# Optimization experiments

Hardware: AMD Instinct MI355X
Metric: run time of the kernel (lower is better)

The kernel has to match this reference:

```python
import jax, jax.numpy as jnp
import numpy as np

B, S, NX, NH = 4, 1024, 1024, 16
HD = NX // NH  # head_features = 64


def setup_inputs() -> dict:
    key = jax.random.key(0)
    k1, k2, k3 = jax.random.split(key, 3)
    x = jax.random.normal(k1, (B, S, NX), dtype=jnp.float32)
    w_attn = 0.02 * jax.random.normal(k2, (NX, 3 * NX), dtype=jnp.float32)
    b_attn = jnp.zeros((3 * NX,), dtype=jnp.float32)
    w_proj = 0.02 * jax.random.normal(k3, (NX, NX), dtype=jnp.float32)
    b_proj = jnp.zeros((NX,), dtype=jnp.float32)
    causal_bias = jnp.tril(jnp.ones((S, S), dtype=jnp.float32))  # tril buffer
    return {"x": x, "w_attn": w_attn, "b_attn": b_attn,
            "w_proj": w_proj, "b_proj": b_proj, "causal_bias": causal_bias}


def reference(x, w_attn, b_attn, w_proj, b_proj, causal_bias):
    # c_attn: fused qkv projection (Conv1D == addmm)
    qkv = x @ w_attn + b_attn                     # [B, S, 3*NX]
    q, k, v = jnp.split(qkv, 3, axis=-1)          # each [B, S, NX]
    # split heads -> [B, H, S, D]
    q = q.reshape(B, S, NH, HD).transpose(0, 2, 1, 3)
    k = k.reshape(B, S, NH, HD).transpose(0, 2, 1, 3)
    v = v.reshape(B, S, NH, HD).transpose(0, 2, 1, 3)
    # present: stack of (key in [B,H,S,D] layout, value)
    present = jnp.stack((k, v))                   # [2, B, H, S, D]
    # scores with scale=True
    w = jnp.einsum('bhqd,bhkd->bhqk', q, k) / jnp.sqrt(jnp.float32(HD))
    b = causal_bias[None, None, :, :]             # [1,1,S,S] (nd==ns==S)
    w = w * b - 1e10 * (1.0 - b)                  # multiplicative mask trick
    p = jax.nn.softmax(w, axis=-1)
    a = jnp.einsum('bhqk,bhkd->bhqd', p, v)       # [B, H, S, D]
    a = a.transpose(0, 2, 1, 3).reshape(B, S, NX)  # merge heads
    out = a @ w_proj + b_proj                     # c_proj
    return out, present
```

## Files before the change

### kernel.cpp

```cpp
#include <hip/hip_runtime.h>
#include <hip/hip_bf16.h>

typedef __attribute__((ext_vector_type(8))) short short8;
typedef __attribute__((ext_vector_type(4))) float floatx4;

constexpr int Bsz = 4, Ssz = 1024, NXc = 1024, NHc = 16, HDc = 64;
constexpr int OUT_ELEMS  = Bsz * Ssz * NXc;
constexpr int HEAD_ELEMS = Bsz * NHc * Ssz * HDc;

union BF8 { __hip_bfloat16 h[8]; uint4 v; short8 s; };

__device__ __forceinline__ uint4 cvt8(const float* __restrict__ p) {
    float4 a = *reinterpret_cast<const float4*>(p);
    float4 b = *reinterpret_cast<const float4*>(p + 4);
    BF8 u;
    u.h[0] = __float2bfloat16(a.x); u.h[1] = __float2bfloat16(a.y);
    u.h[2] = __float2bfloat16(a.z); u.h[3] = __float2bfloat16(a.w);
    u.h[4] = __float2bfloat16(b.x); u.h[5] = __float2bfloat16(b.y);
    u.h[6] = __float2bfloat16(b.z); u.h[7] = __float2bfloat16(b.w);
    return u.v;
}

__device__ __forceinline__ void load_lds_16B(const void* g, void* l) {
    __builtin_amdgcn_global_load_lds(
        (const __attribute__((address_space(1))) unsigned int*)g,
        (__attribute__((address_space(3))) unsigned int*)l, 16, 0, 0);
}


__global__ __launch_bounds__(256) void prep_kernel(
    const float* __restrict__ x, __hip_bfloat16* __restrict__ x_bf,
    const float* __restrict__ w_attn, __hip_bfloat16* __restrict__ wTa,
    const float* __restrict__ w_proj, __hip_bfloat16* __restrict__ wTp)
{
    const int bid = blockIdx.x, tid = threadIdx.x;
    __shared__ float t[64][65];
    if (bid < 2048) {
        const int i = (bid * 256 + tid) * 8;
        *reinterpret_cast<uint4*>(x_bf + i) = cvt8(x + i);
        return;
    }
    const float* in; __hip_bfloat16* outp; int N, bx, by;
    if (bid < 2816) { const int q = bid - 2048; in = w_attn; outp = wTa; N = 3072; bx = q % 48; by = q / 48; }
    else            { const int q = bid - 2816; in = w_proj; outp = wTp; N = 1024; bx = q % 16; by = q / 16; }
    const int k0 = by * 64, n0 = bx * 64;
#pragma unroll
    for (int j = 0; j < 16; ++j) {
        const int idx = tid + j * 256;
        const int row = idx >> 6, col = idx & 63;
        t[row][col] = in[(size_t)(k0 + row) * N + n0 + col];
    }
    __syncthreads();
#pragma unroll
    for (int j = 0; j < 16; ++j) {
        const int idx = tid + j * 256;
        const int orow = idx >> 6, ocol = idx & 63;
        outp[(size_t)(n0 + orow) * 1024 + k0 + ocol] = __float2bfloat16(t[ocol][orow]);
    }
}

template <int EPI>
__global__ __launch_bounds__(256) void gemm128p(
    const __hip_bfloat16* __restrict__ A,
    const __hip_bfloat16* __restrict__ Bt,
    const float* __restrict__ bias,
    float* __restrict__ outf,
    __hip_bfloat16* __restrict__ qws,
    float* __restrict__ present,
    __hip_bfloat16* __restrict__ kws,
    __hip_bfloat16* __restrict__ vtws,
    int M, int N, int K)
{
    __shared__ __align__(16) __hip_bfloat16 As[3][4096];
    __shared__ __align__(16) __hip_bfloat16 Bs[3][4096];

    const int nbx = N >> 7;
    const int nwg = (M >> 7) * nbx;
    const int wg  = blockIdx.x;
    const int swz = (wg & 7) * (nwg >> 3) + (wg >> 3);
    const int by  = swz / nbx, bx = swz % nbx;

    const int tid  = threadIdx.x;
    const int w    = tid >> 6, lane = tid & 63;
    const int quad = lane >> 4, l16 = lane & 15;
    const int m0 = by * 128, n0 = bx * 128;
    const int mb = (w >> 1) * 64, nbw = (w & 1) * 64;

    const int srow = lane >> 2;
    const int sksw = (((lane & 3) ^ ((lane >> 3) & 3))) * 8;
    const int rsw = (l16 >> 1) & 3;

    floatx4 acc[4][4];
#pragma unroll
    for (int i = 0; i < 4; ++i)
#pragma unroll
        for (int j = 0; j < 4; ++j)
#pragma unroll
            for (int r = 0; r < 4; ++r) acc[i][j][r] = 0.f;

    auto stage = [&](int buf, int k0) {
#pragma unroll
        for (int c = 0; c < 2; ++c) {
            const int chunk = w * 2 + c;
            const int row = chunk * 16 + srow;
            load_lds_16B(A + (size_t)(m0 + row) * K + k0 + sksw,
                         &As[buf][chunk * 512]);
            load_lds_16B(Bt + (size_t)(n0 + row) * K + k0 + sksw,
                         &Bs[buf][chunk * 512]);
        }
    };

    stage(0, 0);
    stage(1, 32);
    int cb = 0;
    for (int k0 = 0; k0 < K; k0 += 32) {
        if (k0 + 32 < K) {
            asm volatile("s_waitcnt vmcnt(4)" ::: "memory");
        } else {
            asm volatile("s_waitcnt vmcnt(0)" ::: "memory");
        }
        __builtin_amdgcn_s_barrier();
        __builtin_amdgcn_sched_barrier(0);

        if (k0 + 64 < K) {
            const int nb_ = (cb >= 1) ? cb - 1 : 2;
            stage(nb_, k0 + 64);
        }

        short8 af[4], bfr[4];
#pragma unroll
        for (int mi = 0; mi < 4; ++mi)
            af[mi] = *reinterpret_cast<const short8*>(
                &As[cb][(mb + mi * 16 + l16) * 32 + ((quad ^ rsw) * 8)]);
#pragma unroll
        for (int ni = 0; ni < 4; ++ni)
            bfr[ni] = *reinterpret_cast<const short8*>(
                &Bs[cb][(nbw + ni * 16 + l16) * 32 + ((quad ^ rsw) * 8)]);
        __builtin_amdgcn_s_setprio(1);
#pragma unroll
        for (int mi = 0; mi < 4; ++mi)
#pragma unroll
            for (int ni = 0; ni < 4; ++ni)
                acc[mi][ni] = __builtin_amdgcn_mfma_f32_16x16x32_bf16(
                    af[mi], bfr[ni], acc[mi][ni], 0, 0, 0);
        __builtin_amdgcn_s_setprio(0);

        cb = (cb == 2) ? 0 : cb + 1;
    }

#pragma unroll
    for (int mi = 0; mi < 4; ++mi) {
#pragma unroll
        for (int ni = 0; ni < 4; ++ni) {
            const int col = n0 + nbw + ni * 16 + l16;
            const float bsv = bias[col];
#pragma unroll
            for (int r = 0; r < 4; ++r) {
                const int row = m0 + mb + mi * 16 + quad * 4 + r;
                const float v = acc[mi][ni][r] + bsv;
                if (EPI == 0) {
                    const int seg = col >> 10;
                    const int c = col & 1023;
                    if (seg == 0) {
                        qws[(size_t)row * 1024 + c] = __float2bfloat16(v);
                    } else {
                        const int bq = row >> 10, s = row & 1023;
                        const int hh = c >> 6, d = c & 63;
                        const size_t idx =
                            ((size_t)((bq * 16 + hh) * 1024 + s)) * 64 + d;
                        const int kt = s >> 6, key = s & 63;
                        const size_t tbase =
                            ((size_t)((bq * 16 + hh) * 16 + kt)) * 4096;
                        if (seg == 1) {
                            present[idx] = v;
                            kws[tbase + key * 64 +
                                ((((d >> 3) ^ (key & 7)) << 3) | (d & 7))] =
                                __float2bfloat16(v);
                        } else {
                            present[HEAD_ELEMS + idx] = v;
                            vtws[tbase + d * 64 +
                                ((((key >> 3) ^ (d & 7)) << 3) | (key & 7))] =
                                __float2bfloat16(v);
                        }
                    }
                } else {
                    outf[(size_t)row * N + col] = v;
                }
            }
        }
    }
}

__global__ __launch_bounds__(256) void gemm_proj(
    const __hip_bfloat16* __restrict__ A,
    const __hip_bfloat16* __restrict__ Bt,
    const float* __restrict__ bias,
    float* __restrict__ outf)
{
    constexpr int K = 1024, N = 1024;
    __shared__ __align__(16) __hip_bfloat16 As[3][4096];
    __shared__ __align__(16) __hip_bfloat16 Bs[3][2048];

    const int wg  = blockIdx.x;
    const int swz = (wg & 7) * 64 + (wg >> 3);
    const int by  = swz >> 4, bx = swz & 15;

    const int tid  = threadIdx.x;
    const int w    = tid >> 6, lane = tid & 63;
    const int quad = lane >> 4, l16 = lane & 15;
    const int m0 = by * 128, n0 = bx * 64;
    const int mbase = w * 32;

    const int srow = lane >> 2;
    const int sksw = (((lane & 3) ^ ((lane >> 3) & 3))) * 8;
    const int rsw = (l16 >> 1) & 3;

    floatx4 acc[2][4];
#pragma unroll
    for (int i = 0; i < 2; ++i)
#pragma unroll
        for (int j = 0; j < 4; ++j)
#pragma unroll
            for (int r = 0; r < 4; ++r) acc[i][j][r] = 0.f;

    auto stage = [&](int buf, int k0) {
#pragma unroll
        for (int c = 0; c < 2; ++c) {
            const int chunk = w * 2 + c;
            const int row = chunk * 16 + srow;
            load_lds_16B(A + (size_t)(m0 + row) * K + k0 + sksw,
                         &As[buf][chunk * 512]);
        }
        const int brow = w * 16 + srow;
        load_lds_16B(Bt + (size_t)(n0 + brow) * K + k0 + sksw,
                     &Bs[buf][w * 512]);
    };

    stage(0, 0);
    stage(1, 32);
    int cb = 0;
    for (int k0 = 0; k0 < K; k0 += 32) {
        if (k0 + 32 < K) {
            asm volatile("s_waitcnt vmcnt(3)" ::: "memory");
        } else {
            asm volatile("s_waitcnt vmcnt(0)" ::: "memory");
        }
        __builtin_amdgcn_s_barrier();
        __builtin_amdgcn_sched_barrier(0);

        if (k0 + 64 < K) {
            const int nb_ = (cb >= 1) ? cb - 1 : 2;
            stage(nb_, k0 + 64);
        }

        short8 af[2], bfr[4];
#pragma unroll
        for (int mi = 0; mi < 2; ++mi)
            af[mi] = *reinterpret_cast<const short8*>(
                &As[cb][(mbase + mi * 16 + l16) * 32 + ((quad ^ rsw) * 8)]);
#pragma unroll
        for (int ni = 0; ni < 4; ++ni)
            bfr[ni] = *reinterpret_cast<const short8*>(
                &Bs[cb][(ni * 16 + l16) * 32 + ((quad ^ rsw) * 8)]);
        __builtin_amdgcn_s_setprio(1);
#pragma unroll
        for (int mi = 0; mi < 2; ++mi)
#pragma unroll
            for (int ni = 0; ni < 4; ++ni)
                acc[mi][ni] = __builtin_amdgcn_mfma_f32_16x16x32_bf16(
                    af[mi], bfr[ni], acc[mi][ni], 0, 0, 0);
        __builtin_amdgcn_s_setprio(0);

        cb = (cb == 2) ? 0 : cb + 1;
    }

#pragma unroll
    for (int mi = 0; mi < 2; ++mi) {
#pragma unroll
        for (int ni = 0; ni < 4; ++ni) {
            const int col = n0 + ni * 16 + l16;
            const float bsv = bias[col];
#pragma unroll
            for (int r = 0; r < 4; ++r) {
                const int row = m0 + mbase + mi * 16 + quad * 4 + r;
                outf[(size_t)row * N + col] = acc[mi][ni][r] + bsv;
            }
        }
    }
}

__global__ __launch_bounds__(256) void attn_v6(
    const __hip_bfloat16* __restrict__ q_ws,
    const __hip_bfloat16* __restrict__ k_ws,
    const __hip_bfloat16* __restrict__ vt_ws,
    __hip_bfloat16* __restrict__ a_ws)
{
    const int wg  = blockIdx.x;
    const int swz = (wg & 7) * 64 + (wg >> 3);
    const int bx  = swz & 7;
    const int bh  = swz >> 3;
    const int b = bh >> 4, h = bh & 15;

    const int tid  = threadIdx.x;
    const int wave = tid >> 6, lane = tid & 63;
    const int quad = lane >> 4, l16 = lane & 15;
    const int stripe = wave * 16;

    const __hip_bfloat16* Kbase = k_ws  + (size_t)bh * 65536;
    const __hip_bfloat16* Vbase = vt_ws + (size_t)bh * 65536;

    __shared__ __align__(16) __hip_bfloat16 Ksf[4][4096];
    __shared__ __align__(16) __hip_bfloat16 Vsf[4][4096];
    __shared__ __align__(16) __hip_bfloat16 Ps[64][72];

    constexpr float SCL = 0.18033688011f;

#pragma unroll
    for (int pass = 0; pass < 2; ++pass) {
        const int qt = (pass == 0) ? (8 + bx) : (7 - bx);

        const __hip_bfloat16* Qb =
            q_ws + ((size_t)(b * Ssz + qt * 64 + stripe + l16)) * NXc + h * 64;
        const short8 qf0 = *reinterpret_cast<const short8*>(Qb + quad * 8);
        const short8 qf1 = *reinterpret_cast<const short8*>(Qb + 32 + quad * 8);

        float m_i[4], l_i[4];
#pragma unroll
        for (int r = 0; r < 4; ++r) { m_i[r] = -1e9f; l_i[r] = 0.f; }
        floatx4 oacc[4];
#pragma unroll
        for (int ni = 0; ni < 4; ++ni)
#pragma unroll
            for (int r = 0; r < 4; ++r) oacc[ni][r] = 0.f;

#pragma unroll
        for (int c2 = 0; c2 < 2; ++c2) {
            const int c = wave + c2 * 4;
            load_lds_16B(Kbase + c * 512 + (lane << 3), &Ksf[0][c * 512]);
            load_lds_16B(Vbase + c * 512 + (lane << 3), &Vsf[0][c * 512]);
        }
        if (qt >= 1) {
#pragma unroll
            for (int c2 = 0; c2 < 2; ++c2) {
                const int c = wave + c2 * 4;
                load_lds_16B(Kbase + 4096 + c * 512 + (lane << 3),
                             &Ksf[1][c * 512]);
                load_lds_16B(Vbase + 4096 + c * 512 + (lane << 3),
                             &Vsf[1][c * 512]);
            }
        }

        for (int kt = 0; kt <= qt; ++kt) {
            const int cw = kt & 3;
            if (kt + 2 <= qt) {
                const int nb_ = (kt + 2) & 3;
                const __hip_bfloat16* Kt = Kbase + (size_t)(kt + 2) * 4096;
                const __hip_bfloat16* Vt = Vbase + (size_t)(kt + 2) * 4096;
#pragma unroll
                for (int c2 = 0; c2 < 2; ++c2) {
                    const int c = wave + c2 * 4;
                    load_lds_16B(Kt + c * 512 + (lane << 3), &Ksf[nb_][c * 512]);
                    load_lds_16B(Vt + c * 512 + (lane << 3), &Vsf[nb_][c * 512]);
                }
                asm volatile("s_waitcnt vmcnt(8)" ::: "memory");
            } else if (kt + 1 <= qt) {
                asm volatile("s_waitcnt vmcnt(4)" ::: "memory");
            } else {
                asm volatile("s_waitcnt vmcnt(0)" ::: "memory");
            }
            __builtin_amdgcn_s_barrier();
            __builtin_amdgcn_sched_barrier(0);

            floatx4 sacc[4];
#pragma unroll
            for (int ni = 0; ni < 4; ++ni)
#pragma unroll
                for (int r = 0; r < 4; ++r) sacc[ni][r] = 0.f;
            __builtin_amdgcn_s_setprio(1);
#pragma unroll
            for (int ni = 0; ni < 4; ++ni) {
                const int key = ni * 16 + l16;
                const int sw = key & 7;
                const short8 kf0 = *reinterpret_cast<const short8*>(
                    &Ksf[cw][key * 64 + ((quad ^ sw) << 3)]);
                const short8 kf1 = *reinterpret_cast<const short8*>(
                    &Ksf[cw][key * 64 + (((4 + quad) ^ sw) << 3)]);
                sacc[ni] = __builtin_amdgcn_mfma_f32_16x16x32_bf16(
                    qf0, kf0, sacc[ni], 0, 0, 0);
                sacc[ni] = __builtin_amdgcn_mfma_f32_16x16x32_bf16(
                    qf1, kf1, sacc[ni], 0, 0, 0);
            }
            __builtin_amdgcn_s_setprio(0);

            const bool diag = (kt == qt);
            float alpha_[4];
#pragma unroll
            for (int r = 0; r < 4; ++r) {
                const int lrow = stripe + quad * 4 + r;
                float sv[4];
                float mx = -1e30f;
#pragma unroll
                for (int ni = 0; ni < 4; ++ni) {
                    float v = sacc[ni][r] * SCL;
                    if (diag && (ni * 16 + l16) > lrow) v = -1e9f;
                    sv[ni] = v;
                    mx = fmaxf(mx, v);
                }
                mx = fmaxf(mx, __shfl_xor(mx, 1));
                mx = fmaxf(mx, __shfl_xor(mx, 2));
                mx = fmaxf(mx, __shfl_xor(mx, 4));
                mx = fmaxf(mx, __shfl_xor(mx, 8));
                const float mnew = fmaxf(m_i[r], mx);
                const float al = exp2f(m_i[r] - mnew);
                m_i[r] = mnew;
                float s = 0.f;
#pragma unroll
                for (int nn = 0; nn < 4; ++nn) {
                    const int ni = (nn + quad) & 3;
                    const float p = exp2f(sv[ni] - mnew);
                    s += p;
                    Ps[lrow][ni * 16 + l16] = __float2bfloat16(p);
                }
                s += __shfl_xor(s, 1);
                s += __shfl_xor(s, 2);
                s += __shfl_xor(s, 4);
                s += __shfl_xor(s, 8);
                l_i[r] = l_i[r] * al + s;
                alpha_[r] = al;
            }

#pragma unroll
            for (int ni = 0; ni < 4; ++ni)
#pragma unroll
                for (int r = 0; r < 4; ++r) oacc[ni][r] *= alpha_[r];

            __builtin_amdgcn_s_setprio(1);
#pragma unroll
            for (int kk = 0; kk < 64; kk += 32) {
                const short8 pf = *reinterpret_cast<const short8*>(
                    &Ps[stripe + l16][kk + quad * 8]);
#pragma unroll
                for (int ni = 0; ni < 4; ++ni) {
                    const int d = ni * 16 + l16;
                    const int chunk = (kk >> 3) + quad;
                    const short8 vf = *reinterpret_cast<const short8*>(
                        &Vsf[cw][d * 64 + ((chunk ^ (d & 7)) << 3)]);
                    oacc[ni] = __builtin_amdgcn_mfma_f32_16x16x32_bf16(
                        pf, vf, oacc[ni], 0, 0, 0);
                }
            }
            __builtin_amdgcn_s_setprio(0);
        }

        __builtin_amdgcn_s_barrier();

#pragma unroll
        for (int ni = 0; ni < 4; ++ni) {
#pragma unroll
            for (int r = 0; r < 4; ++r) {
                const int row = qt * 64 + stripe + quad * 4 + r;
                const int col = h * 64 + ni * 16 + l16;
                const float inv = 1.0f / fmaxf(l_i[r], 1e-20f);
                a_ws[((size_t)(b * Ssz + row)) * NXc + col] =
                    __float2bfloat16(oacc[ni][r] * inv);
            }
        }
    }
}

template <int EPI>
__global__ __launch_bounds__(256) void gemm64(
    const void* __restrict__ Av, const float* __restrict__ Bw,
    const float* __restrict__ bias, float* __restrict__ out0,
    float* __restrict__ present, int M, int N, int K)
{
    __shared__ __align__(16) __hip_bfloat16 As[64][40];
    __shared__ __align__(16) __hip_bfloat16 Bs[64][40];
    const int tid = threadIdx.x;
    const int wave = tid >> 6, lane = tid & 63;
    const int quad = lane >> 4, l16 = lane & 15;
    const int m0 = blockIdx.y * 64, n0 = blockIdx.x * 64;
    const int mb = (wave >> 1) * 32, nb = (wave & 1) * 32;
    const int arow = tid >> 2, aseg = tid & 3;
    const int brow = tid >> 3, bseg = tid & 7;
    floatx4 acc[2][2];
#pragma unroll
    for (int i = 0; i < 2; ++i)
#pragma unroll
        for (int j = 0; j < 2; ++j)
#pragma unroll
            for (int r = 0; r < 4; ++r) acc[i][j][r] = 0.f;
    for (int k0 = 0; k0 < K; k0 += 32) {
        if (EPI == 0) {
            const float* A = (const float*)Av;
            *reinterpret_cast<uint4*>(&As[arow][aseg * 8]) =
                cvt8(A + (size_t)(m0 + arow) * K + k0 + aseg * 8);
        } else {
            const __hip_bfloat16* A = (const __hip_bfloat16*)Av;
            *reinterpret_cast<uint4*>(&As[arow][aseg * 8]) =
                *reinterpret_cast<const uint4*>(
                    A + (size_t)(m0 + arow) * K + k0 + aseg * 8);
        }
        const float* bp = Bw + (size_t)(k0 + brow) * N + n0 + bseg * 8;
        float4 b0 = *reinterpret_cast<const float4*>(bp);
        float4 b1 = *reinterpret_cast<const float4*>(bp + 4);
        Bs[bseg * 8 + 0][brow] = __float2bfloat16(b0.x);
        Bs[bseg * 8 + 1][brow] = __float2bfloat16(b0.y);
        Bs[bseg * 8 + 2][brow] = __float2bfloat16(b0.z);
        Bs[bseg * 8 + 3][brow] = __float2bfloat16(b0.w);
        Bs[bseg * 8 + 4][brow] = __float2bfloat16(b1.x);
        Bs[bseg * 8 + 5][brow] = __float2bfloat16(b1.y);
        Bs[bseg * 8 + 6][brow] = __float2bfloat16(b1.z);
        Bs[bseg * 8 + 7][brow] = __float2bfloat16(b1.w);
        __syncthreads();
        short8 af[2], bf[2];
#pragma unroll
        for (int mm = 0; mm < 2; ++mm)
            af[mm] = *reinterpret_cast<const short8*>(&As[mb + mm * 16 + l16][quad * 8]);
#pragma unroll
        for (int nn = 0; nn < 2; ++nn)
            bf[nn] = *reinterpret_cast<const short8*>(&Bs[nb + nn * 16 + l16][quad * 8]);
#pragma unroll
        for (int mm = 0; mm < 2; ++mm)
#pragma unroll
            for (int nn = 0; nn < 2; ++nn)
                acc[mm][nn] = __builtin_amdgcn_mfma_f32_16x16x32_bf16(
                    af[mm], bf[nn], acc[mm][nn], 0, 0, 0);
        __syncthreads();
    }
#pragma unroll
    for (int mm = 0; mm < 2; ++mm)
#pragma unroll
        for (int nn = 0; nn < 2; ++nn) {
            const int col = n0 + nb + nn * 16 + l16;
            const float bsv = bias[col];
#pragma unroll
            for (int r = 0; r < 4; ++r) {
                const int row = m0 + mb + mm * 16 + quad * 4 + r;
                const float v = acc[mm][nn][r] + bsv;
                if (EPI == 0) {
                    const int seg = col >> 10;
                    const int c = col & 1023;
                    if (seg == 0) out0[(size_t)row * 1024 + c] = v;
                    else {
                        const int b = row >> 10, s = row & 1023;
                        const int h = c >> 6, d = c & 63;
                        const size_t idx = ((size_t)((b * 16 + h) * 1024 + s)) * 64 + d;
                        if (seg == 1) present[idx] = v;
                        else          present[HEAD_ELEMS + idx] = v;
                    }
                } else out0[(size_t)row * N + col] = v;
            }
        }
}

__global__ __launch_bounds__(256) void attn64(
    const float* __restrict__ qbuf, const float* __restrict__ present,
    __hip_bfloat16* __restrict__ a_ws)
{
    const int qt = blockIdx.x, h = blockIdx.y, b = blockIdx.z;
    const int tid = threadIdx.x;
    const int wave = tid >> 6, lane = tid & 63;
    const int quad = lane >> 4, l16 = lane & 15;
    const int mb = (wave >> 1) * 32, nb = (wave & 1) * 32;
    const size_t headoff = ((size_t)(b * 16 + h)) * Ssz * HDc;
    const float* Qb = qbuf + ((size_t)(b * Ssz + qt * 64)) * NXc + h * 64;
    const float* Kp = present + headoff;
    const float* Vp = present + HEAD_ELEMS + headoff;
    __shared__ __align__(16) __hip_bfloat16 Qs[64][72];
    __shared__ __align__(16) __hip_bfloat16 Ks[64][72];
    __shared__ __align__(16) __hip_bfloat16 Vts[64][72];
    __shared__ __align__(16) __hip_bfloat16 Ps[64][72];
    __shared__ float Sc[64][65];
    __shared__ float mrow[64], lrow[64], arw[64];
#pragma unroll
    for (int it = 0; it < 2; ++it) {
        const int c = tid + it * 256;
        const int row = c >> 3, seg = c & 7;
        *reinterpret_cast<uint4*>(&Qs[row][seg * 8]) =
            cvt8(Qb + (size_t)row * NXc + seg * 8);
    }
    if (tid < 64) { mrow[tid] = -1e9f; lrow[tid] = 0.f; }
    floatx4 oacc[2][2];
#pragma unroll
    for (int i = 0; i < 2; ++i)
#pragma unroll
        for (int j = 0; j < 2; ++j)
#pragma unroll
            for (int r = 0; r < 4; ++r) oacc[i][j][r] = 0.f;
    __syncthreads();
    for (int kt = 0; kt <= qt; ++kt) {
#pragma unroll
        for (int it = 0; it < 2; ++it) {
            const int c = tid + it * 256;
            const int row = c >> 3, seg = c & 7;
            *reinterpret_cast<uint4*>(&Ks[row][seg * 8]) =
                cvt8(Kp + (size_t)(kt * 64 + row) * 64 + seg * 8);
            const float* vp = Vp + (size_t)(kt * 64 + row) * 64 + seg * 8;
            float4 v0 = *reinterpret_cast<const float4*>(vp);
            float4 v1 = *reinterpret_cast<const float4*>(vp + 4);
            Vts[seg * 8 + 0][row] = __float2bfloat16(v0.x);
            Vts[seg * 8 + 1][row] = __float2bfloat16(v0.y);
            Vts[seg * 8 + 2][row] = __float2bfloat16(v0.z);
            Vts[seg * 8 + 3][row] = __float2bfloat16(v0.w);
            Vts[seg * 8 + 4][row] = __float2bfloat16(v1.x);
            Vts[seg * 8 + 5][row] = __float2bfloat16(v1.y);
            Vts[seg * 8 + 6][row] = __float2bfloat16(v1.z);
            Vts[seg * 8 + 7][row] = __float2bfloat16(v1.w);
        }
        __syncthreads();
        floatx4 sacc[2][2];
#pragma unroll
        for (int i = 0; i < 2; ++i)
#pragma unroll
            for (int j = 0; j < 2; ++j)
#pragma unroll
                for (int r = 0; r < 4; ++r) sacc[i][j][r] = 0.f;
#pragma unroll
        for (int kd = 0; kd < 64; kd += 32) {
            short8 af[2], bf[2];
#pragma unroll
            for (int mm = 0; mm < 2; ++mm)
                af[mm] = *reinterpret_cast<const short8*>(&Qs[mb + mm * 16 + l16][kd + quad * 8]);
#pragma unroll
            for (int nn = 0; nn < 2; ++nn)
                bf[nn] = *reinterpret_cast<const short8*>(&Ks[nb + nn * 16 + l16][kd + quad * 8]);
#pragma unroll
            for (int mm = 0; mm < 2; ++mm)
#pragma unroll
                for (int nn = 0; nn < 2; ++nn)
                    sacc[mm][nn] = __builtin_amdgcn_mfma_f32_16x16x32_bf16(
                        af[mm], bf[nn], sacc[mm][nn], 0, 0, 0);
        }
        const bool diag = (kt == qt);
#pragma unroll
        for (int mm = 0; mm < 2; ++mm)
#pragma unroll
            for (int nn = 0; nn < 2; ++nn)
#pragma unroll
                for (int r = 0; r < 4; ++r) {
                    const int row = mb + mm * 16 + quad * 4 + r;
                    const int col = nb + nn * 16 + l16;
                    float v = fminf(fmaxf(sacc[mm][nn][r] * 0.125f, -1e8f), 1e8f);
                    if (diag && col > row) v = -1e9f;
                    Sc[row][col] = v;
                }
        __syncthreads();
        if (tid < 64) {
            const int r = tid;
            const float mo = mrow[r];
            float mx = mo;
            for (int c = 0; c < 64; ++c) mx = fmaxf(mx, Sc[r][c]);
            const float al = (mo <= -5e8f) ? 0.f : __expf(mo - mx);
            float sum = 0.f;
            for (int c = 0; c < 64; ++c) {
                const float sv = Sc[r][c];
                const float p = (sv <= -5e8f) ? 0.f : __expf(sv - mx);
                sum += p;
                Ps[r][c] = __float2bfloat16(p);
            }
            mrow[r] = mx;
            lrow[r] = lrow[r] * al + sum;
            arw[r]  = al;
        }
        __syncthreads();
#pragma unroll
        for (int mm = 0; mm < 2; ++mm) {
            const int rbase = mb + mm * 16 + quad * 4;
#pragma unroll
            for (int r = 0; r < 4; ++r) {
                const float al = arw[rbase + r];
                oacc[mm][0][r] *= al;
                oacc[mm][1][r] *= al;
            }
        }
#pragma unroll
        for (int kk = 0; kk < 64; kk += 32) {
            short8 pf[2], vf[2];
#pragma unroll
            for (int mm = 0; mm < 2; ++mm)
                pf[mm] = *reinterpret_cast<const short8*>(&Ps[mb + mm * 16 + l16][kk + quad * 8]);
#pragma unroll
            for (int nn = 0; nn < 2; ++nn)
                vf[nn] = *reinterpret_cast<const short8*>(&Vts[nb + nn * 16 + l16][kk + quad * 8]);
#pragma unroll
            for (int mm = 0; mm < 2; ++mm)
#pragma unroll
                for (int nn = 0; nn < 2; ++nn)
                    oacc[mm][nn] = __builtin_amdgcn_mfma_f32_16x16x32_bf16(
                        pf[mm], vf[nn], oacc[mm][nn], 0, 0, 0);
        }
        __syncthreads();
    }
#pragma unroll
    for (int mm = 0; mm < 2; ++mm)
#pragma unroll
        for (int nn = 0; nn < 2; ++nn)
#pragma unroll
            for (int r = 0; r < 4; ++r) {
                const int row = mb + mm * 16 + quad * 4 + r;
                const int col = nb + nn * 16 + l16;
                const float inv = 1.0f / fmaxf(lrow[row], 1e-20f);
                a_ws[((size_t)(b * Ssz + qt * 64 + row)) * NXc + h * 64 + col] =
                    __float2bfloat16(oacc[mm][nn][r] * inv);
            }
}

extern "C" void kernel_launch(void* const* d_in, const int* in_sizes, int n_in,
                              void* d_out, int out_size, void* d_ws, size_t ws_size,
                              hipStream_t stream) {
    const float* x      = (const float*)d_in[0];
    const float* w_attn = (const float*)d_in[1];
    const float* b_attn = (const float*)d_in[2];
    const float* w_proj = (const float*)d_in[3];
    const float* b_proj = (const float*)d_in[4];

    float* out     = (float*)d_out;
    float* present = out + OUT_ELEMS;

    const size_t NEED = 32u * 1024u * 1024u;
    if (ws_size >= NEED) {
        __hip_bfloat16* reg1 = (__hip_bfloat16*)d_ws;
        __hip_bfloat16* reg2 = reg1 + 4194304;
        __hip_bfloat16* reg3 = reg2 + 4194304;
        __hip_bfloat16* wTa  = reg3 + 4194304;
        __hip_bfloat16* wTp  = wTa + 3145728;
        __hip_bfloat16* kws  = (__hip_bfloat16*)out;
        __hip_bfloat16* vtws = kws + 4194304;

        prep_kernel<<<3072, 256, 0, stream>>>(x, reg1, w_attn, wTa, w_proj, wTp);

        gemm128p<0><<<768, 256, 0, stream>>>(
            reg1, wTa, b_attn, nullptr, reg2, present, kws, vtws,
            4096, 3072, 1024);

        attn_v6<<<512, 256, 0, stream>>>(reg2, kws, vtws, reg2);

        gemm_proj<<<512, 256, 0, stream>>>(reg2, wTp, b_proj, out);
    } else {
        __hip_bfloat16* a_ws = (__hip_bfloat16*)d_ws;
        hipMemsetAsync(d_ws, 0, (size_t)OUT_ELEMS * sizeof(__hip_bfloat16), stream);
        gemm64<0><<<dim3(48, 64), 256, 0, stream>>>(x, w_attn, b_attn, out, present,
                                                    4096, 3072, 1024);
        attn64<<<dim3(16, 16, 4), 256, 0, stream>>>(out, present, a_ws);
        gemm64<1><<<dim3(16, 64), 256, 0, stream>>>(a_ws, w_proj, b_proj, out, nullptr,
                                                    4096, 1024, 1024);
    }
}
```

Measured before the change: 195.9 us.

## Replace QKV GEMM with 256x256-tile, 8-wave kernel and split-phase staging

The QKV projection GEMM moves from 128x128 tiles with 4 waves to 256x256 tiles with 8 waves, each wave computing 128x64. Each K-step is split into two MFMA halves, with the A and B prefetches interleaved between barriers. The aim is more operand reuse per LDS load and better overlap of global-to-LDS traffic with MFMA work. The grid shrinks from 768 to 192 workgroups, which is fewer than the CU count on MI355X, so occupancy and load balance may suffer, and LDS use rises to 96KB per block.

```diff
diff --git a/kernel.cpp b/kernel.cpp
--- a/kernel.cpp
+++ b/kernel.cpp
@@ -59,132 +59,155 @@
     }
 }
 
-template <int EPI>
-__global__ __launch_bounds__(256) void gemm128p(
+__global__ __launch_bounds__(512) void gemm256(
     const __hip_bfloat16* __restrict__ A,
     const __hip_bfloat16* __restrict__ Bt,
     const float* __restrict__ bias,
-    float* __restrict__ outf,
     __hip_bfloat16* __restrict__ qws,
     float* __restrict__ present,
     __hip_bfloat16* __restrict__ kws,
-    __hip_bfloat16* __restrict__ vtws,
-    int M, int N, int K)
+    __hip_bfloat16* __restrict__ vtws)
 {
-    __shared__ __align__(16) __hip_bfloat16 As[3][4096];
-    __shared__ __align__(16) __hip_bfloat16 Bs[3][4096];
-
-    const int nbx = N >> 7;
-    const int nwg = (M >> 7) * nbx;
+    constexpr int K = 1024;
+    __shared__ __align__(16) __hip_bfloat16 As[3][8192];
+    __shared__ __align__(16) __hip_bfloat16 Bs[3][8192];
+
     const int wg  = blockIdx.x;
-    const int swz = (wg & 7) * (nwg >> 3) + (wg >> 3);
-    const int by  = swz / nbx, bx = swz % nbx;
+    const int swz = (wg & 7) * 24 + (wg >> 3);
+    const int by  = swz / 12, bx = swz % 12;
 
     const int tid  = threadIdx.x;
     const int w    = tid >> 6, lane = tid & 63;
+    const int wm   = w >> 2, wn = w & 3;
     const int quad = lane >> 4, l16 = lane & 15;
-    const int m0 = by * 128, n0 = bx * 128;
-    const int mb = (w >> 1) * 64, nbw = (w & 1) * 64;
+    const int m0 = by * 256, n0 = bx * 256;
+    const int mb = wm * 128, nb = wn * 64;
 
     const int srow = lane >> 2;
-    const int sksw = (((lane & 3) ^ ((lane >> 3) & 3))) * 8;
-    const int rsw = (l16 >> 1) & 3;
-
-    floatx4 acc[4][4];
-#pragma unroll
-    for (int i = 0; i < 4; ++i)
+    const int sk   = (((lane & 3) ^ ((lane >> 3) & 3))) * 8;
+    const int rsw  = (l16 >> 1) & 3;
+
+    floatx4 acc[8][4];
+#pragma unroll
+    for (int i = 0; i < 8; ++i)
 #pragma unroll
         for (int j = 0; j < 4; ++j)
 #pragma unroll
             for (int r = 0; r < 4; ++r) acc[i][j][r] = 0.f;
 
-    auto stage = [&](int buf, int k0) {
+    auto stageA = [&](int buf, int k0) {
 #pragma unroll
         for (int c = 0; c < 2; ++c) {
-            const int chunk = w * 2 + c;
-            const int row = chunk * 16 + srow;
-            load_lds_16B(A + (size_t)(m0 + row) * K + k0 + sksw,
-                         &As[buf][chunk * 512]);
-            load_lds_16B(Bt + (size_t)(n0 + row) * K + k0 + sksw,
-                         &Bs[buf][chunk * 512]);
+            const int blk = w * 2 + c;
+            const int row = blk * 16 + srow;
+            load_lds_16B(A + (size_t)(m0 + row) * K + k0 + sk,
+                         &As[buf][blk * 512]);
         }
     };
-
-    stage(0, 0);
-    stage(1, 32);
-    int cb = 0;
-    for (int k0 = 0; k0 < K; k0 += 32) {
-        if (k0 + 32 < K) {
+    auto stageB = [&](int buf, int k0) {
+#pragma unroll
+        for (int c = 0; c < 2; ++c) {
+            const int blk = w * 2 + c;
+            const int row = blk * 16 + srow;
+            load_lds_16B(Bt + (size_t)(n0 + row) * K + k0 + sk,
+                         &Bs[buf][blk * 512]);
+        }
+    };
+
+    stageA(0, 0);  stageB(0, 0);
+    stageA(1, 32); stageB(1, 32);
+    asm volatile("s_waitcnt vmcnt(4)" ::: "memory");
+    __builtin_amdgcn_s_barrier();
+    __builtin_amdgcn_sched_barrier(0);
+
+    for (int t = 0; t < 32; ++t) {
+        const int cb = t % 3;
+        const int k0 = t * 32;
+        const int nbuf = (t + 2) % 3;
+        const int rc = (quad ^ rsw) * 8;
+
+        short8 af0[4], bfr[4];
+#pragma unroll
+        for (int mi = 0; mi < 4; ++mi)
+            af0[mi] = *reinterpret_cast<const short8*>(
+                &As[cb][(mb + mi * 16 + l16) * 32 + rc]);
+#pragma unroll
+        for (int ni = 0; ni < 4; ++ni)
+            bfr[ni] = *reinterpret_cast<const short8*>(
+                &Bs[cb][(nb + ni * 16 + l16) * 32 + rc]);
+        if (t + 2 < 32) stageA(nbuf, k0 + 64);
+        __builtin_amdgcn_s_barrier();
+        __builtin_amdgcn_sched_barrier(0);
+        __builtin_amdgcn_s_setprio(1);
+#pragma unroll
+        for (int mi = 0; mi < 4; ++mi)
+#pragma unroll
+            for (int ni = 0; ni < 4; ++ni)
+                acc[mi][ni] = __builtin_amdgcn_mfma_f32_16x16x32_bf16(
+                    af0[mi], bfr[ni], acc[mi][ni], 0, 0, 0);
+        __builtin_amdgcn_s_setprio(0);
+
+        short8 af1[4];
+#pragma unroll
+        for (int mi = 0; mi < 4; ++mi)
+            af1[mi] = *reinterpret_cast<const short8*>(
+                &As[cb][(mb + 64 + mi * 16 + l16) * 32 + rc]);
+        if (t + 2 < 32) stageB(nbuf, k0 + 64);
+        __builtin_amdgcn_s_barrier();
+        __builtin_amdgcn_sched_barrier(0);
+        __builtin_amdgcn_s_setprio(1);
+#pragma unroll
+        for (int mi = 0; mi < 4; ++mi)
+#pragma unroll
+            for (int ni = 0; ni < 4; ++ni)
+                acc[4 + mi][ni] = __builtin_amdgcn_mfma_f32_16x16x32_bf16(
+                    af1[mi], bfr[ni], acc[4 + mi][ni], 0, 0, 0);
+        __builtin_amdgcn_s_setprio(0);
+
+        if (t + 2 < 32) {
             asm volatile("s_waitcnt vmcnt(4)" ::: "memory");
         } else {
             asm volatile("s_waitcnt vmcnt(0)" ::: "memory");
         }
-        __builtin_amdgcn_s_barrier();
-        __builtin_amdgcn_sched_barrier(0);
-
-        if (k0 + 64 < K) {
-            const int nb_ = (cb >= 1) ? cb - 1 : 2;
-            stage(nb_, k0 + 64);
-        }
-
-        short8 af[4], bfr[4];
-#pragma unroll
-        for (int mi = 0; mi < 4; ++mi)
-            af[mi] = *reinterpret_cast<const short8*>(
-                &As[cb][(mb + mi * 16 + l16) * 32 + ((quad ^ rsw) * 8)]);
-#pragma unroll
-        for (int ni = 0; ni < 4; ++ni)
-            bfr[ni] = *reinterpret_cast<const short8*>(
-                &Bs[cb][(nbw + ni * 16 + l16) * 32 + ((quad ^ rsw) * 8)]);
-        __builtin_amdgcn_s_setprio(1);
-#pragma unroll
-        for (int mi = 0; mi < 4; ++mi)
-#pragma unroll
-            for (int ni = 0; ni < 4; ++ni)
-                acc[mi][ni] = __builtin_amdgcn_mfma_f32_16x16x32_bf16(
-                    af[mi], bfr[ni], acc[mi][ni], 0, 0, 0);
-        __builtin_amdgcn_s_setprio(0);
-
-        cb = (cb == 2) ? 0 : cb + 1;
-    }
-
-#pragma unroll
-    for (int mi = 0; mi < 4; ++mi) {
+        if (t < 31) {
+            __builtin_amdgcn_s_barrier();
+            __builtin_amdgcn_sched_barrier(0);
+        }
+    }
+
+#pragma unroll
+    for (int mi = 0; mi < 8; ++mi) {
 #pragma unroll
         for (int ni = 0; ni < 4; ++ni) {
-            const int col = n0 + nbw + ni * 16 + l16;
+            const int col = n0 + nb + ni * 16 + l16;
             const float bsv = bias[col];
 #pragma unroll
             for (int r = 0; r < 4; ++r) {
                 const int row = m0 + mb + mi * 16 + quad * 4 + r;
                 const float v = acc[mi][ni][r] + bsv;
-                if (EPI == 0) {
-                    const int seg = col >> 10;
-                    const int c = col & 1023;
-                    if (seg == 0) {
-                        qws[(size_t)row * 1024 + c] = __float2bfloat16(v);
+                const int seg = col >> 10;
+                const int c = col & 1023;
+                if (seg == 0) {
+                    qws[(size_t)row * 1024 + c] = __float2bfloat16(v);
+                } else {
+                    const int bq = row >> 10, s = row & 1023;
+                    const int hh = c >> 6, d = c & 63;
+                    const size_t idx =
+                        ((size_t)((bq * 16 + hh) * 1024 + s)) * 64 + d;
+                    const int kt = s >> 6, key = s & 63;
+                    const size_t tbase =
+                        ((size_t)((bq * 16 + hh) * 16 + kt)) * 4096;
+                    if (seg == 1) {
+                        present[idx] = v;
+                        kws[tbase + key * 64 +
+                            ((((d >> 3) ^ (key & 7)) << 3) | (d & 7))] =
+                            __float2bfloat16(v);
                     } else {
-                        const int bq = row >> 10, s = row & 1023;
-                        const int hh = c >> 6, d = c & 63;
-                        const size_t idx =
-                            ((size_t)((bq * 16 + hh) * 1024 + s)) * 64 + d;
-                        const int kt = s >> 6, key = s & 63;
-                        const size_t tbase =
-                            ((size_t)((bq * 16 + hh) * 16 + kt)) * 4096;
-                        if (seg == 1) {
-                            present[idx] = v;
-                            kws[tbase + key * 64 +
-                                ((((d >> 3) ^ (key & 7)) << 3) | (d & 7))] =
-                                __float2bfloat16(v);
-                        } else {
-                            present[HEAD_ELEMS + idx] = v;
-                            vtws[tbase + d * 64 +
-                                ((((key >> 3) ^ (d & 7)) << 3) | (key & 7))] =
-                                __float2bfloat16(v);
-                        }
+                        present[HEAD_ELEMS + idx] = v;
+                        vtws[tbase + d * 64 +
+                            ((((key >> 3) ^ (d & 7)) << 3) | (key & 7))] =
+                            __float2bfloat16(v);
                     }
-                } else {
-                    outf[(size_t)row * N + col] = v;
                 }
             }
         }
@@ -730,9 +753,8 @@
 
         prep_kernel<<<3072, 256, 0, stream>>>(x, reg1, w_attn, wTa, w_proj, wTp);
 
-        gemm128p<0><<<768, 256, 0, stream>>>(
-            reg1, wTa, b_attn, nullptr, reg2, present, kws, vtws,
-            4096, 3072, 1024);
+        gemm256<<<192, 512, 0, stream>>>(
+            reg1, wTa, b_attn, reg2, present, kws, vtws);
 
         attn_v6<<<512, 256, 0, stream>>>(reg2, kws, vtws, reg2);
 
```

After: 203.8 us. 4.0% more time.

## Fuse fp32-to-bf16 conversion of x into QKV GEMM A-operand loads

Applied to the files above, without the earlier changes.

Removes the separate x-to-bf16 conversion pass from the prep kernel. The QKV GEMM now reads fp32 activations straight from global memory into registers, converts them to bf16 fragments, and prefetches one k-step ahead, while B still goes through LDS with global_load_lds. This saves one write and one read of a 16 MB bf16 copy of x. In exchange the GEMM reads twice as many A bytes, since fp32 is re-read by each N-tile block without LDS sharing, and the vmcnt accounting becomes more delicate.

```diff
diff --git a/kernel.cpp b/kernel.cpp
--- a/kernel.cpp
+++ b/kernel.cpp
@@ -21,6 +21,15 @@
     return u.v;
 }
 
+__device__ __forceinline__ short8 cvt8r(const float4& a, const float4& b) {
+    BF8 u;
+    u.h[0] = __float2bfloat16(a.x); u.h[1] = __float2bfloat16(a.y);
+    u.h[2] = __float2bfloat16(a.z); u.h[3] = __float2bfloat16(a.w);
+    u.h[4] = __float2bfloat16(b.x); u.h[5] = __float2bfloat16(b.y);
+    u.h[6] = __float2bfloat16(b.z); u.h[7] = __float2bfloat16(b.w);
+    return u.s;
+}
+
 __device__ __forceinline__ void load_lds_16B(const void* g, void* l) {
     __builtin_amdgcn_global_load_lds(
         (const __attribute__((address_space(1))) unsigned int*)g,
@@ -29,20 +38,14 @@
 
 
 __global__ __launch_bounds__(256) void prep_kernel(
-    const float* __restrict__ x, __hip_bfloat16* __restrict__ x_bf,
     const float* __restrict__ w_attn, __hip_bfloat16* __restrict__ wTa,
     const float* __restrict__ w_proj, __hip_bfloat16* __restrict__ wTp)
 {
     const int bid = blockIdx.x, tid = threadIdx.x;
     __shared__ float t[64][65];
-    if (bid < 2048) {
-        const int i = (bid * 256 + tid) * 8;
-        *reinterpret_cast<uint4*>(x_bf + i) = cvt8(x + i);
-        return;
-    }
     const float* in; __hip_bfloat16* outp; int N, bx, by;
-    if (bid < 2816) { const int q = bid - 2048; in = w_attn; outp = wTa; N = 3072; bx = q % 48; by = q / 48; }
-    else            { const int q = bid - 2816; in = w_proj; outp = wTp; N = 1024; bx = q % 16; by = q / 16; }
+    if (bid < 768) { in = w_attn; outp = wTa; N = 3072; bx = bid % 48; by = bid / 48; }
+    else { const int q = bid - 768; in = w_proj; outp = wTp; N = 1024; bx = q % 16; by = q / 16; }
     const int k0 = by * 64, n0 = bx * 64;
 #pragma unroll
     for (int j = 0; j < 16; ++j) {
@@ -59,19 +62,16 @@
     }
 }
 
-template <int EPI>
-__global__ __launch_bounds__(256) void gemm128p(
-    const __hip_bfloat16* __restrict__ A,
+__global__ __launch_bounds__(256) void gemm_qkv(
+    const float* __restrict__ A,
     const __hip_bfloat16* __restrict__ Bt,
     const float* __restrict__ bias,
-    float* __restrict__ outf,
     __hip_bfloat16* __restrict__ qws,
     float* __restrict__ present,
     __hip_bfloat16* __restrict__ kws,
-    __hip_bfloat16* __restrict__ vtws,
-    int M, int N, int K)
+    __hip_bfloat16* __restrict__ vtws)
 {
-    __shared__ __align__(16) __hip_bfloat16 As[3][4096];
+    constexpr int M = 4096, N = 3072, K = 1024;
     __shared__ __align__(16) __hip_bfloat16 Bs[3][4096];
 
     const int nbx = N >> 7;
@@ -88,7 +88,7 @@
 
     const int srow = lane >> 2;
     const int sksw = (((lane & 3) ^ ((lane >> 3) & 3))) * 8;
-    const int rsw = (l16 >> 1) & 3;
+    const int rsw  = (l16 >> 1) & 3;
 
     floatx4 acc[4][4];
 #pragma unroll
@@ -98,40 +98,51 @@
 #pragma unroll
             for (int r = 0; r < 4; ++r) acc[i][j][r] = 0.f;
 
-    auto stage = [&](int buf, int k0) {
+    auto stageB = [&](int buf, int k0) {
 #pragma unroll
         for (int c = 0; c < 2; ++c) {
             const int chunk = w * 2 + c;
             const int row = chunk * 16 + srow;
-            load_lds_16B(A + (size_t)(m0 + row) * K + k0 + sksw,
-                         &As[buf][chunk * 512]);
             load_lds_16B(Bt + (size_t)(n0 + row) * K + k0 + sksw,
                          &Bs[buf][chunk * 512]);
         }
     };
 
-    stage(0, 0);
-    stage(1, 32);
-    int cb = 0;
-    for (int k0 = 0; k0 < K; k0 += 32) {
-        if (k0 + 32 < K) {
-            asm volatile("s_waitcnt vmcnt(4)" ::: "memory");
+    const float* Ab = A + (size_t)(m0 + mb + l16) * K + quad * 8;
+
+    float4 an0[4], an1[4];
+    auto loadA = [&](int k0) {
+#pragma unroll
+        for (int mi = 0; mi < 4; ++mi) {
+            const float* p = Ab + (size_t)(mi * 16) * K + k0;
+            an0[mi] = *reinterpret_cast<const float4*>(p);
+            an1[mi] = *reinterpret_cast<const float4*>(p + 4);
+        }
+    };
+
+    loadA(0);
+    stageB(0, 0);
+    stageB(1, 32);
+
+    for (int t = 0; t < 32; ++t) {
+        const int cb = t % 3;
+        if (t < 31) {
+            asm volatile("s_waitcnt vmcnt(10)" ::: "memory");
         } else {
-            asm volatile("s_waitcnt vmcnt(0)" ::: "memory");
+            asm volatile("s_waitcnt vmcnt(8)" ::: "memory");
         }
         __builtin_amdgcn_s_barrier();
         __builtin_amdgcn_sched_barrier(0);
 
-        if (k0 + 64 < K) {
-            const int nb_ = (cb >= 1) ? cb - 1 : 2;
-            stage(nb_, k0 + 64);
-        }
-
-        short8 af[4], bfr[4];
+        short8 af[4];
 #pragma unroll
         for (int mi = 0; mi < 4; ++mi)
-            af[mi] = *reinterpret_cast<const short8*>(
-                &As[cb][(mb + mi * 16 + l16) * 32 + ((quad ^ rsw) * 8)]);
+            af[mi] = cvt8r(an0[mi], an1[mi]);
+
+        if (t + 1 < 32) loadA((t + 1) * 32);
+        if (t + 2 < 32) stageB((t + 2) % 3, (t + 2) * 32);
+
+        short8 bfr[4];
 #pragma unroll
         for (int ni = 0; ni < 4; ++ni)
             bfr[ni] = *reinterpret_cast<const short8*>(
@@ -144,8 +155,6 @@
                 acc[mi][ni] = __builtin_amdgcn_mfma_f32_16x16x32_bf16(
                     af[mi], bfr[ni], acc[mi][ni], 0, 0, 0);
         __builtin_amdgcn_s_setprio(0);
-
-        cb = (cb == 2) ? 0 : cb + 1;
     }
 
 #pragma unroll
@@ -158,33 +167,29 @@
             for (int r = 0; r < 4; ++r) {
                 const int row = m0 + mb + mi * 16 + quad * 4 + r;
                 const float v = acc[mi][ni][r] + bsv;
-                if (EPI == 0) {
-                    const int seg = col >> 10;
-                    const int c = col & 1023;
-                    if (seg == 0) {
-                        qws[(size_t)row * 1024 + c] = __float2bfloat16(v);
+                const int seg = col >> 10;
+                const int c = col & 1023;
+                if (seg == 0) {
+                    qws[(size_t)row * 1024 + c] = __float2bfloat16(v);
+                } else {
+                    const int bq = row >> 10, s = row & 1023;
+                    const int hh = c >> 6, d = c & 63;
+                    const size_t idx =
+                        ((size_t)((bq * 16 + hh) * 1024 + s)) * 64 + d;
+                    const int kt = s >> 6, key = s & 63;
+                    const size_t tbase =
+                        ((size_t)((bq * 16 + hh) * 16 + kt)) * 4096;
+                    if (seg == 1) {
+                        present[idx] = v;
+                        kws[tbase + key * 64 +
+                            ((((d >> 3) ^ (key & 7)) << 3) | (d & 7))] =
+                            __float2bfloat16(v);
                     } else {
-                        const int bq = row >> 10, s = row & 1023;
-                        const int hh = c >> 6, d = c & 63;
-                        const size_t idx =
-                            ((size_t)((bq * 16 + hh) * 1024 + s)) * 64 + d;
-                        const int kt = s >> 6, key = s & 63;
-                        const size_t tbase =
-                            ((size_t)((bq * 16 + hh) * 16 + kt)) * 4096;
-                        if (seg == 1) {
-                            present[idx] = v;
-                            kws[tbase + key * 64 +
-                                ((((d >> 3) ^ (key & 7)) << 3) | (d & 7))] =
-                                __float2bfloat16(v);
-                        } else {
-                            present[HEAD_ELEMS + idx] = v;
-                            vtws[tbase + d * 64 +
-                                ((((key >> 3) ^ (d & 7)) << 3) | (key & 7))] =
-                                __float2bfloat16(v);
-                        }
+                        present[HEAD_ELEMS + idx] = v;
+                        vtws[tbase + d * 64 +
+                            ((((key >> 3) ^ (d & 7)) << 3) | (key & 7))] =
+                            __float2bfloat16(v);
                     }
-                } else {
-                    outf[(size_t)row * N + col] = v;
                 }
             }
         }
@@ -728,11 +733,10 @@
         __hip_bfloat16* kws  = (__hip_bfloat16*)out;
         __hip_bfloat16* vtws = kws + 4194304;
 
-        prep_kernel<<<3072, 256, 0, stream>>>(x, reg1, w_attn, wTa, w_proj, wTp);
-
-        gemm128p<0><<<768, 256, 0, stream>>>(
-            reg1, wTa, b_attn, nullptr, reg2, present, kws, vtws,
-            4096, 3072, 1024);
+        prep_kernel<<<1024, 256, 0, stream>>>(w_attn, wTa, w_proj, wTp);
+
+        gemm_qkv<<<768, 256, 0, stream>>>(
+            x, wTa, b_attn, reg2, present, kws, vtws);
 
         attn_v6<<<512, 256, 0, stream>>>(reg2, kws, vtws, reg2);
 
```

After: 285.2 us. 45.6% more time.
